# Performance work log

Hardware: AMD Instinct MI355X
Metric: run time of the kernel (lower is better)

Reference implementation:

```python
import jax, jax.numpy as jnp
import numpy as np

BATCH, IN_F, OUT_F = 4096, 1024, 1024


def setup_inputs() -> dict:
    key = jax.random.key(0)
    kx, kw = jax.random.split(key)
    x = jax.random.normal(kx, (BATCH, IN_F, 4), dtype=jnp.float32)
    weight = jax.random.normal(kw, (OUT_F, IN_F, 4), dtype=jnp.float32) * 0.01
    bias = jnp.zeros((OUT_F, 4), dtype=jnp.float32)
    return {"x": x, "weight": weight, "bias": bias}


def reference(x, weight, bias):
    # x: (batch, in, 4) quaternions; weight: (out, in, 4); bias: (out, 4)
    # Hamilton product broadcast over (batch, out, in) then summed over in ==
    # 16 signed real GEMMs contracting the `in` dimension.
    ar, ai, aj, ak = x[..., 0], x[..., 1], x[..., 2], x[..., 3]          # (b, i)
    br, bi, bj, bk = weight[..., 0], weight[..., 1], weight[..., 2], weight[..., 3]  # (o, i)

    mm = lambda a, w: jnp.einsum('bi,oi->bo', a, w)

    out_r = mm(ar, br) - mm(ai, bi) - mm(aj, bj) - mm(ak, bk)
    out_i = mm(ar, bi) + mm(ai, br) + mm(aj, bk) - mm(ak, bj)
    out_j = mm(ar, bj) - mm(ai, bk) + mm(aj, br) + mm(ak, bi)
    out_k = mm(ar, bk) + mm(ai, bj) - mm(aj, bi) + mm(ak, br)

    out = jnp.stack([out_r, out_i, out_j, out_k], axis=-1)  # (b, o, 4)
    return out + bias
```

## Files before the change

kernel.cpp:

```cpp
#include <hip/hip_runtime.h>


typedef __bf16 bf16x8 __attribute__((ext_vector_type(8)));
typedef float floatx4 __attribute__((ext_vector_type(4)));

constexpr int M = 4096;
constexpr int N = 4096;
constexpr int K = 4096;
constexpr int BM = 256, BN = 256, BK = 64;
constexpr int TILES = K / BK;

constexpr int CVT_BLOCKS = (M * K / 8) / 256;
constexpr int EXP_BLOCKS = (1024 * 1024 / 2) / 256;

#define BARRIER() asm volatile("s_barrier" ::: "memory")
#define SB()      __builtin_amdgcn_sched_barrier(0)
#define LGKM0()   do { asm volatile("s_waitcnt lgkmcnt(0)"); SB(); } while (0)
#define LGKM4()   do { asm volatile("s_waitcnt lgkmcnt(4)"); SB(); } while (0)
#define LDS_OFF(p) ((unsigned)(uintptr_t)(__attribute__((address_space(3))) const void*)(p))

__global__ void prep_kernel(const float* __restrict__ x, const float* __restrict__ w,
                            __bf16* __restrict__ A, __bf16* __restrict__ Wb) {
    const int b = blockIdx.x;
    if (b < CVT_BLOCKS) {
        const size_t i = (size_t)b * 256 + threadIdx.x;
        const float4* xp = (const float4*)x;
        float4 a = xp[2 * i];
        float4 c = xp[2 * i + 1];
        bf16x8 v;
        v[0] = (__bf16)a.x; v[1] = (__bf16)a.y; v[2] = (__bf16)a.z; v[3] = (__bf16)a.w;
        v[4] = (__bf16)c.x; v[5] = (__bf16)c.y; v[6] = (__bf16)c.z; v[7] = (__bf16)c.w;
        *(bf16x8*)(A + 8 * i) = v;
    } else {
        const int idx = (b - CVT_BLOCKS) * 256 + threadIdx.x;
        const int o  = idx >> 9;
        const int ip = (idx & 511) * 2;
        float4 q0 = ((const float4*)w)[o * 1024 + ip];
        float4 q1 = ((const float4*)w)[o * 1024 + ip + 1];
        __bf16* base = Wb + (size_t)(o * 4) * K + ip * 4;
        bf16x8 r;
        r[0] = (__bf16)q0.x; r[1] = (__bf16)(-q0.y); r[2] = (__bf16)(-q0.z); r[3] = (__bf16)(-q0.w);
        r[4] = (__bf16)q1.x; r[5] = (__bf16)(-q1.y); r[6] = (__bf16)(-q1.z); r[7] = (__bf16)(-q1.w);
        *(bf16x8*)(base) = r;
        r[0] = (__bf16)q0.y; r[1] = (__bf16)q0.x; r[2] = (__bf16)q0.w; r[3] = (__bf16)(-q0.z);
        r[4] = (__bf16)q1.y; r[5] = (__bf16)q1.x; r[6] = (__bf16)q1.w; r[7] = (__bf16)(-q1.z);
        *(bf16x8*)(base + (size_t)K) = r;
        r[0] = (__bf16)q0.z; r[1] = (__bf16)(-q0.w); r[2] = (__bf16)q0.x; r[3] = (__bf16)q0.y;
        r[4] = (__bf16)q1.z; r[5] = (__bf16)(-q1.w); r[6] = (__bf16)q1.x; r[7] = (__bf16)q1.y;
        *(bf16x8*)(base + (size_t)2 * K) = r;
        r[0] = (__bf16)q0.w; r[1] = (__bf16)q0.z; r[2] = (__bf16)(-q0.y); r[3] = (__bf16)q0.x;
        r[4] = (__bf16)q1.w; r[5] = (__bf16)q1.z; r[6] = (__bf16)(-q1.y); r[7] = (__bf16)q1.x;
        *(bf16x8*)(base + (size_t)3 * K) = r;
    }
}

__device__ __forceinline__ void gload_lds16(const __bf16* g, __bf16* l) {
    __builtin_amdgcn_global_load_lds(
        (const __attribute__((address_space(1))) void*)g,
        (__attribute__((address_space(3))) void*)l, 16, 0, 0);
}

__device__ __forceinline__ bf16x8 dsr128(unsigned addr) {
    bf16x8 r;
    asm volatile("ds_read_b128 %0, %1" : "=v"(r) : "v"(addr));
    return r;
}

__global__ __launch_bounds__(512, 2) void qgemm_kernel(const __bf16* __restrict__ A,
                                                       const __bf16* __restrict__ B,
                                                       const float* __restrict__ bias,
                                                       float* __restrict__ C) {
    __shared__ __bf16 As[2][BM][BK];
    __shared__ __bf16 Bs[2][BN][BK];

    const int tid  = threadIdx.x;
    const int wave = tid >> 6;
    const int lane = tid & 63;

    const int bid = blockIdx.x;
    const int xcd = bid & 7;
    const int q   = bid >> 3;
    const int tm  = (xcd >> 2) * 8 + (q & 7);
    const int tn  = (xcd & 3) * 4 + (q >> 3);
    const int bm  = tm * BM;
    const int bn  = tn * BN;

    const int wm = (wave >> 2) * 128;
    const int wn = (wave & 3) * 64;

    const int srow = wave * 16 + (lane >> 3);
    const int schk = ((lane & 7) ^ (lane >> 3)) * 8;
    const __bf16* agA = A + (size_t)(bm + srow) * K + schk;
    const __bf16* agB = B + (size_t)(bn + srow) * K + schk;

    auto issueA = [&](int buf, int h, int t) {
        const __bf16* g = agA + (size_t)h * 128 * K + t * BK;
        gload_lds16(g,                 &As[buf][h * 128 + wave * 16][0]);
        gload_lds16(g + (size_t)8 * K, &As[buf][h * 128 + wave * 16 + 8][0]);
    };
    auto issueB = [&](int buf, int h, int t) {
        const __bf16* g = agB + (size_t)h * 128 * K + t * BK;
        gload_lds16(g,                 &Bs[buf][h * 128 + wave * 16][0]);
        gload_lds16(g + (size_t)8 * K, &Bs[buf][h * 128 + wave * 16 + 8][0]);
    };

    const int fl  = lane & 15;
    const int fq  = lane >> 4;
    const int fx7 = fl & 7;
    const unsigned ebo0 = (unsigned)(((fq)     ^ fx7) * 16);
    const unsigned ebo1 = (unsigned)(((4 + fq) ^ fx7) * 16);
    const unsigned aRow = LDS_OFF(&As[0][0][0]) + (unsigned)(wm + fl) * 128u;
    const unsigned bRow = LDS_OFF(&Bs[0][0][0]) + (unsigned)(wn + fl) * 128u;

    floatx4 acc[8][4] = {};
    bf16x8 x0, x1, x2, x3, y0, y1, y2, y3;
    bf16x8 bE0, bE1, bE2, bE3, bO0, bO1, bO2, bO3;
    bf16x8 s0, s1, s2, s3;

#define HALF(i0, i1, AA, AB, F0, F1, F2, F3)                                      \
    acc[i0][0] = __builtin_amdgcn_mfma_f32_16x16x32_bf16(AA, F0, acc[i0][0], 0, 0, 0); \
    acc[i1][0] = __builtin_amdgcn_mfma_f32_16x16x32_bf16(AB, F0, acc[i1][0], 0, 0, 0); \
    acc[i0][1] = __builtin_amdgcn_mfma_f32_16x16x32_bf16(AA, F1, acc[i0][1], 0, 0, 0); \
    acc[i1][1] = __builtin_amdgcn_mfma_f32_16x16x32_bf16(AB, F1, acc[i1][1], 0, 0, 0); \
    acc[i0][2] = __builtin_amdgcn_mfma_f32_16x16x32_bf16(AA, F2, acc[i0][2], 0, 0, 0); \
    acc[i1][2] = __builtin_amdgcn_mfma_f32_16x16x32_bf16(AB, F2, acc[i1][2], 0, 0, 0); \
    acc[i0][3] = __builtin_amdgcn_mfma_f32_16x16x32_bf16(AA, F3, acc[i0][3], 0, 0, 0); \
    acc[i1][3] = __builtin_amdgcn_mfma_f32_16x16x32_bf16(AB, F3, acc[i1][3], 0, 0, 0)

#define TILE(T, BUFC, BC0, BC1, BC2, BC3, BX0, BX1, BX2, BX3, ISSB)               \
    do {                                                                          \
        const unsigned bsc_ = (BUFC) * 32768u;                                    \
        const unsigned bsn_ = (1 - (BUFC)) * 32768u;                              \
                \
        issueA(1 - (BUFC), 0, (T) + 1); issueA(1 - (BUFC), 1, (T) + 1);           \
        s0 = dsr128(bRow + bsc_ + 0u    + ebo1);                                  \
        s1 = dsr128(bRow + bsc_ + 2048u + ebo1);                                  \
        s2 = dsr128(bRow + bsc_ + 4096u + ebo1);                                  \
        s3 = dsr128(bRow + bsc_ + 6144u + ebo1);                                  \
        y0 = dsr128(aRow + bsc_ + 4096u + ebo0);                                  \
        y1 = dsr128(aRow + bsc_ + 4096u + ebo1);                                  \
        y2 = dsr128(aRow + bsc_ + 6144u + ebo0);                                  \
        y3 = dsr128(aRow + bsc_ + 6144u + ebo1);                                  \
        SB();                                                                     \
        __builtin_amdgcn_s_setprio(1);                                            \
        HALF(0, 1, x0, x2, BC0, BC1, BC2, BC3);                                   \
        __builtin_amdgcn_s_setprio(0);                                            \
        LGKM4();                                    \
        __builtin_amdgcn_s_setprio(1);                                            \
        HALF(0, 1, x1, x3, s0, s1, s2, s3);                                       \
        __builtin_amdgcn_s_setprio(0);                                            \
        LGKM0();                                                                  \
              \
        x0 = dsr128(aRow + bsc_ + 8192u  + ebo0);                                 \
        x1 = dsr128(aRow + bsc_ + 8192u  + ebo1);                                 \
        x2 = dsr128(aRow + bsc_ + 10240u + ebo0);                                 \
        x3 = dsr128(aRow + bsc_ + 10240u + ebo1);                                 \
        SB();                                                                     \
        __builtin_amdgcn_s_setprio(1);                                            \
        HALF(2, 3, y0, y2, BC0, BC1, BC2, BC3);                                   \
        HALF(2, 3, y1, y3, s0, s1, s2, s3);                                       \
        __builtin_amdgcn_s_setprio(0);                                            \
        LGKM0();                                                                  \
        asm volatile("s_waitcnt vmcnt(0)");       \
        BARRIER();                                        \
        if (ISSB) { issueB((BUFC), 0, (T) + 2); issueB((BUFC), 1, (T) + 2); }     \
                 \
        y0 = dsr128(aRow + bsc_ + 12288u + ebo0);                                 \
        y1 = dsr128(aRow + bsc_ + 12288u + ebo1);                                 \
        y2 = dsr128(aRow + bsc_ + 14336u + ebo0);                                 \
        y3 = dsr128(aRow + bsc_ + 14336u + ebo1);                                 \
        BX0 = dsr128(bRow + bsn_ + 0u    + ebo0);                                 \
        BX1 = dsr128(bRow + bsn_ + 2048u + ebo0);                                 \
        BX2 = dsr128(bRow + bsn_ + 4096u + ebo0);                                 \
        BX3 = dsr128(bRow + bsn_ + 6144u + ebo0);                                 \
        SB();                                                                     \
        __builtin_amdgcn_s_setprio(1);                                            \
        HALF(4, 5, x0, x2, BC0, BC1, BC2, BC3);                                   \
        HALF(4, 5, x1, x3, s0, s1, s2, s3);                                       \
        __builtin_amdgcn_s_setprio(0);                                            \
        LGKM4();                                   \
                            \
        x0 = dsr128(aRow + bsn_ + 0u    + ebo0);                                  \
        x1 = dsr128(aRow + bsn_ + 0u    + ebo1);                                  \
        x2 = dsr128(aRow + bsn_ + 2048u + ebo0);                                  \
        x3 = dsr128(aRow + bsn_ + 2048u + ebo1);                                  \
        SB();                                                                     \
        __builtin_amdgcn_s_setprio(1);                                            \
        HALF(6, 7, y0, y2, BC0, BC1, BC2, BC3);                                   \
        HALF(6, 7, y1, y3, s0, s1, s2, s3);                                       \
        __builtin_amdgcn_s_setprio(0);                                            \
        LGKM0();                                         \
        BARRIER();                               \
    } while (0)

    issueB(0, 0, 0); issueB(0, 1, 0);
    issueA(0, 0, 0); issueA(0, 1, 0);
    issueB(1, 0, 1); issueB(1, 1, 1);
    asm volatile("s_waitcnt vmcnt(4)");
    BARRIER();
    bE0 = dsr128(bRow + 0u    + ebo0);
    bE1 = dsr128(bRow + 2048u + ebo0);
    bE2 = dsr128(bRow + 4096u + ebo0);
    bE3 = dsr128(bRow + 6144u + ebo0);
    x0  = dsr128(aRow + 0u    + ebo0);
    x1  = dsr128(aRow + 0u    + ebo1);
    x2  = dsr128(aRow + 2048u + ebo0);
    x3  = dsr128(aRow + 2048u + ebo1);
    LGKM0();

    for (int t = 0; t < 62; t += 2) {
        TILE(t,     0, bE0, bE1, bE2, bE3, bO0, bO1, bO2, bO3, true);
        TILE(t + 1, 1, bO0, bO1, bO2, bO3, bE0, bE1, bE2, bE3, true);
    }
    TILE(62, 0, bE0, bE1, bE2, bE3, bO0, bO1, bO2, bO3, false);

    {
        const unsigned bsc_ = 32768u;
        s0 = dsr128(bRow + bsc_ + 0u    + ebo1);
        s1 = dsr128(bRow + bsc_ + 2048u + ebo1);
        s2 = dsr128(bRow + bsc_ + 4096u + ebo1);
        s3 = dsr128(bRow + bsc_ + 6144u + ebo1);
        y0 = dsr128(aRow + bsc_ + 4096u + ebo0);
        y1 = dsr128(aRow + bsc_ + 4096u + ebo1);
        y2 = dsr128(aRow + bsc_ + 6144u + ebo0);
        y3 = dsr128(aRow + bsc_ + 6144u + ebo1);
        SB();
        __builtin_amdgcn_s_setprio(1);
        HALF(0, 1, x0, x2, bO0, bO1, bO2, bO3);
        __builtin_amdgcn_s_setprio(0);
        LGKM4();
        __builtin_amdgcn_s_setprio(1);
        HALF(0, 1, x1, x3, s0, s1, s2, s3);
        __builtin_amdgcn_s_setprio(0);
        LGKM0();
        x0 = dsr128(aRow + bsc_ + 8192u  + ebo0);
        x1 = dsr128(aRow + bsc_ + 8192u  + ebo1);
        x2 = dsr128(aRow + bsc_ + 10240u + ebo0);
        x3 = dsr128(aRow + bsc_ + 10240u + ebo1);
        SB();
        __builtin_amdgcn_s_setprio(1);
        HALF(2, 3, y0, y2, bO0, bO1, bO2, bO3);
        HALF(2, 3, y1, y3, s0, s1, s2, s3);
        __builtin_amdgcn_s_setprio(0);
        LGKM0();
        y0 = dsr128(aRow + bsc_ + 12288u + ebo0);
        y1 = dsr128(aRow + bsc_ + 12288u + ebo1);
        y2 = dsr128(aRow + bsc_ + 14336u + ebo0);
        y3 = dsr128(aRow + bsc_ + 14336u + ebo1);
        SB();
        __builtin_amdgcn_s_setprio(1);
        HALF(4, 5, x0, x2, bO0, bO1, bO2, bO3);
        HALF(4, 5, x1, x3, s0, s1, s2, s3);
        __builtin_amdgcn_s_setprio(0);
        LGKM0();
        __builtin_amdgcn_s_setprio(1);
        HALF(6, 7, y0, y2, bO0, bO1, bO2, bO3);
        HALF(6, 7, y1, y3, s0, s1, s2, s3);
        __builtin_amdgcn_s_setprio(0);
    }

#pragma unroll
    for (int mt = 0; mt < 8; ++mt) {
        const int row = bm + wm + mt * 16 + fq * 4;
#pragma unroll
        for (int nt = 0; nt < 4; ++nt) {
            const int col = bn + wn + nt * 16 + fl;
            const float bv = bias[col];
            float* cp = C + (size_t)row * N + col;
#pragma unroll
            for (int r = 0; r < 4; ++r)
                cp[(size_t)r * N] = acc[mt][nt][r] + bv;
        }
    }
#undef TILE
#undef HALF
}

extern "C" void kernel_launch(void* const* d_in, const int* in_sizes, int n_in,
                              void* d_out, int out_size, void* d_ws, size_t ws_size,
                              hipStream_t stream) {
    const float* x    = (const float*)d_in[0];
    const float* w    = (const float*)d_in[1];
    const float* bias = (const float*)d_in[2];
    float* out = (float*)d_out;

    __bf16* Abf  = (__bf16*)d_ws;
    __bf16* Wbig = (__bf16*)((char*)d_ws + (size_t)M * K * 2);

    prep_kernel<<<CVT_BLOCKS + EXP_BLOCKS, 256, 0, stream>>>(x, w, Abf, Wbig);

    qgemm_kernel<<<256, 512, 0, stream>>>(Abf, Wbig, bias, out);
}
```

Before: 286.5 us.

## Triple-buffer A tiles in LDS with deeper prefetch and immediate-offset LDS reads

Expands the A shared-memory buffer from two stages to three so A tiles are prefetched two iterations ahead. The mid-tile global-load wait becomes a partial vmcnt instead of a full drain, so loads can stay in flight across the barrier. LDS reads now use the ds_read immediate offset field on precomputed per-buffer base addresses, which cuts per-read address arithmetic. The main loop is unrolled by six to rotate the buffers, at the cost of more LDS (160KB per block) and more live VGPRs.

```diff
diff --git a/kernel.cpp b/kernel.cpp
--- a/kernel.cpp
+++ b/kernel.cpp
@@ -8,7 +8,6 @@
 constexpr int N = 4096;
 constexpr int K = 4096;
 constexpr int BM = 256, BN = 256, BK = 64;
-constexpr int TILES = K / BK;
 
 constexpr int CVT_BLOCKS = (M * K / 8) / 256;
 constexpr int EXP_BLOCKS = (1024 * 1024 / 2) / 256;
@@ -60,9 +59,10 @@
         (__attribute__((address_space(3))) void*)l, 16, 0, 0);
 }
 
-__device__ __forceinline__ bf16x8 dsr128(unsigned addr) {
+template <int OFF>
+__device__ __forceinline__ bf16x8 dsrO(unsigned base) {
     bf16x8 r;
-    asm volatile("ds_read_b128 %0, %1" : "=v"(r) : "v"(addr));
+    asm volatile("ds_read_b128 %0, %1 offset:%c2" : "=v"(r) : "v"(base), "i"(OFF));
     return r;
 }
 
@@ -70,7 +70,7 @@
                                                        const __bf16* __restrict__ B,
                                                        const float* __restrict__ bias,
                                                        float* __restrict__ C) {
-    __shared__ __bf16 As[2][BM][BK];
+    __shared__ __bf16 As[3][BM][BK];
     __shared__ __bf16 Bs[2][BN][BK];
 
     const int tid  = threadIdx.x;
@@ -109,15 +109,25 @@
     const int fx7 = fl & 7;
     const unsigned ebo0 = (unsigned)(((fq)     ^ fx7) * 16);
     const unsigned ebo1 = (unsigned)(((4 + fq) ^ fx7) * 16);
-    const unsigned aRow = LDS_OFF(&As[0][0][0]) + (unsigned)(wm + fl) * 128u;
-    const unsigned bRow = LDS_OFF(&Bs[0][0][0]) + (unsigned)(wn + fl) * 128u;
+    const unsigned aR0  = LDS_OFF(&As[0][0][0]) + (unsigned)(wm + fl) * 128u + ebo0;
+    const unsigned aR1  = LDS_OFF(&As[0][0][0]) + (unsigned)(wm + fl) * 128u + ebo1;
+    const unsigned aR0b1 = aR0 + 32768u, aR1b1 = aR1 + 32768u;
+    const unsigned aR0b2 = aR0 + 65536u, aR1b2 = aR1 + 65536u;
+    const unsigned bR0  = LDS_OFF(&Bs[0][0][0]) + (unsigned)(wn + fl) * 128u + ebo0;
+    const unsigned bR1  = LDS_OFF(&Bs[0][0][0]) + (unsigned)(wn + fl) * 128u + ebo1;
+    const unsigned bR0b1 = bR0 + 32768u, bR1b1 = bR1 + 32768u;
 
     floatx4 acc[8][4] = {};
-    bf16x8 x0, x1, x2, x3, y0, y1, y2, y3;
-    bf16x8 bE0, bE1, bE2, bE3, bO0, bO1, bO2, bO3;
+    bf16x8 x0, x1, x2, x3;
+    bf16x8 y0, y1, y2, y3;
+    bf16x8 w0, w1, w2, w3;
+    bf16x8 z0, z1, z2, z3;
     bf16x8 s0, s1, s2, s3;
-
-#define HALF(i0, i1, AA, AB, F0, F1, F2, F3)                                      \
+    bf16x8 c0, c1, c2, c3;
+    bf16x8 d0, d1, d2, d3;
+    bf16x8 n0, n1, n2, n3;
+
+#define HALFK(i0, i1, AA, AB, F0, F1, F2, F3)                                     \
     acc[i0][0] = __builtin_amdgcn_mfma_f32_16x16x32_bf16(AA, F0, acc[i0][0], 0, 0, 0); \
     acc[i1][0] = __builtin_amdgcn_mfma_f32_16x16x32_bf16(AB, F0, acc[i1][0], 0, 0, 0); \
     acc[i0][1] = __builtin_amdgcn_mfma_f32_16x16x32_bf16(AA, F1, acc[i0][1], 0, 0, 0); \
@@ -127,135 +137,117 @@
     acc[i0][3] = __builtin_amdgcn_mfma_f32_16x16x32_bf16(AA, F3, acc[i0][3], 0, 0, 0); \
     acc[i1][3] = __builtin_amdgcn_mfma_f32_16x16x32_bf16(AB, F3, acc[i1][3], 0, 0, 0)
 
-#define TILE(T, BUFC, BC0, BC1, BC2, BC3, BX0, BX1, BX2, BX3, ISSB)               \
+#define TILE(T, A0c, A1c, A0n, A1n, B0c, B1c, B0x, DA, DB, ISSA, ISSB, MIDVM)     \
     do {                                                                          \
-        const unsigned bsc_ = (BUFC) * 32768u;                                    \
-        const unsigned bsn_ = (1 - (BUFC)) * 32768u;                              \
-                \
-        issueA(1 - (BUFC), 0, (T) + 1); issueA(1 - (BUFC), 1, (T) + 1);           \
-        s0 = dsr128(bRow + bsc_ + 0u    + ebo1);                                  \
-        s1 = dsr128(bRow + bsc_ + 2048u + ebo1);                                  \
-        s2 = dsr128(bRow + bsc_ + 4096u + ebo1);                                  \
-        s3 = dsr128(bRow + bsc_ + 6144u + ebo1);                                  \
-        y0 = dsr128(aRow + bsc_ + 4096u + ebo0);                                  \
-        y1 = dsr128(aRow + bsc_ + 4096u + ebo1);                                  \
-        y2 = dsr128(aRow + bsc_ + 6144u + ebo0);                                  \
-        y3 = dsr128(aRow + bsc_ + 6144u + ebo1);                                  \
-        SB();                                                                     \
-        __builtin_amdgcn_s_setprio(1);                                            \
-        HALF(0, 1, x0, x2, BC0, BC1, BC2, BC3);                                   \
-        __builtin_amdgcn_s_setprio(0);                                            \
-        LGKM4();                                    \
-        __builtin_amdgcn_s_setprio(1);                                            \
-        HALF(0, 1, x1, x3, s0, s1, s2, s3);                                       \
-        __builtin_amdgcn_s_setprio(0);                                            \
-        LGKM0();                                                                  \
+                      \
+        if (ISSA) { issueA(DA, 0, (T) + 2); issueA(DA, 1, (T) + 2); }             \
+        s0 = dsrO<0>(B1c); s1 = dsrO<2048>(B1c);                                  \
+        s2 = dsrO<4096>(B1c); s3 = dsrO<6144>(B1c);                               \
+        y0 = dsrO<4096>(A0c); y1 = dsrO<4096>(A1c);                               \
+        y2 = dsrO<6144>(A0c); y3 = dsrO<6144>(A1c);                               \
+        SB();                                                                     \
+        __builtin_amdgcn_s_setprio(1);                                            \
+        HALFK(0, 1, x0, x2, c0, c1, c2, c3);                                      \
+        __builtin_amdgcn_s_setprio(0);                                            \
+        LGKM4();                                       \
+        __builtin_amdgcn_s_setprio(1);                                            \
+        HALFK(0, 1, x1, x3, s0, s1, s2, s3);                                      \
+        __builtin_amdgcn_s_setprio(0);                                            \
+                     \
+        w0 = dsrO<8192>(A0c); w1 = dsrO<8192>(A1c);                               \
+        w2 = dsrO<10240>(A0c); w3 = dsrO<10240>(A1c);                             \
+        SB();                                                                     \
+        LGKM4();                                       \
+        __builtin_amdgcn_s_setprio(1);                                            \
+        HALFK(2, 3, y0, y2, c0, c1, c2, c3);                                      \
+        HALFK(2, 3, y1, y3, s0, s1, s2, s3);                                      \
+        __builtin_amdgcn_s_setprio(0);                                            \
+        LGKM0();                                                      \
+        asm volatile("s_waitcnt vmcnt(" #MIDVM ")");    \
+        BARRIER();                                        \
+        if (ISSB) { issueB(DB, 0, (T) + 2); issueB(DB, 1, (T) + 2); }             \
               \
-        x0 = dsr128(aRow + bsc_ + 8192u  + ebo0);                                 \
-        x1 = dsr128(aRow + bsc_ + 8192u  + ebo1);                                 \
-        x2 = dsr128(aRow + bsc_ + 10240u + ebo0);                                 \
-        x3 = dsr128(aRow + bsc_ + 10240u + ebo1);                                 \
-        SB();                                                                     \
-        __builtin_amdgcn_s_setprio(1);                                            \
-        HALF(2, 3, y0, y2, BC0, BC1, BC2, BC3);                                   \
-        HALF(2, 3, y1, y3, s0, s1, s2, s3);                                       \
-        __builtin_amdgcn_s_setprio(0);                                            \
-        LGKM0();                                                                  \
-        asm volatile("s_waitcnt vmcnt(0)");       \
-        BARRIER();                                        \
-        if (ISSB) { issueB((BUFC), 0, (T) + 2); issueB((BUFC), 1, (T) + 2); }     \
-                 \
-        y0 = dsr128(aRow + bsc_ + 12288u + ebo0);                                 \
-        y1 = dsr128(aRow + bsc_ + 12288u + ebo1);                                 \
-        y2 = dsr128(aRow + bsc_ + 14336u + ebo0);                                 \
-        y3 = dsr128(aRow + bsc_ + 14336u + ebo1);                                 \
-        BX0 = dsr128(bRow + bsn_ + 0u    + ebo0);                                 \
-        BX1 = dsr128(bRow + bsn_ + 2048u + ebo0);                                 \
-        BX2 = dsr128(bRow + bsn_ + 4096u + ebo0);                                 \
-        BX3 = dsr128(bRow + bsn_ + 6144u + ebo0);                                 \
-        SB();                                                                     \
-        __builtin_amdgcn_s_setprio(1);                                            \
-        HALF(4, 5, x0, x2, BC0, BC1, BC2, BC3);                                   \
-        HALF(4, 5, x1, x3, s0, s1, s2, s3);                                       \
-        __builtin_amdgcn_s_setprio(0);                                            \
-        LGKM4();                                   \
-                            \
-        x0 = dsr128(aRow + bsn_ + 0u    + ebo0);                                  \
-        x1 = dsr128(aRow + bsn_ + 0u    + ebo1);                                  \
-        x2 = dsr128(aRow + bsn_ + 2048u + ebo0);                                  \
-        x3 = dsr128(aRow + bsn_ + 2048u + ebo1);                                  \
-        SB();                                                                     \
-        __builtin_amdgcn_s_setprio(1);                                            \
-        HALF(6, 7, y0, y2, BC0, BC1, BC2, BC3);                                   \
-        HALF(6, 7, y1, y3, s0, s1, s2, s3);                                       \
-        __builtin_amdgcn_s_setprio(0);                                            \
-        LGKM0();                                         \
-        BARRIER();                               \
+        z0 = dsrO<12288>(A0c); z1 = dsrO<12288>(A1c);                             \
+        z2 = dsrO<14336>(A0c); z3 = dsrO<14336>(A1c);                             \
+        d0 = dsrO<0>(B0x); d1 = dsrO<2048>(B0x);                                  \
+        d2 = dsrO<4096>(B0x); d3 = dsrO<6144>(B0x);                               \
+        SB();                                                                     \
+        __builtin_amdgcn_s_setprio(1);                                            \
+        HALFK(4, 5, w0, w2, c0, c1, c2, c3);                                      \
+        HALFK(4, 5, w1, w3, s0, s1, s2, s3);                                      \
+        __builtin_amdgcn_s_setprio(0);                                            \
+                                        \
+        LGKM4();                                       \
+        n0 = dsrO<0>(A0n); n1 = dsrO<0>(A1n);                                     \
+        n2 = dsrO<2048>(A0n); n3 = dsrO<2048>(A1n);                               \
+        SB();                                                                     \
+        __builtin_amdgcn_s_setprio(1);                                            \
+        HALFK(6, 7, z0, z2, c0, c1, c2, c3);                                      \
+        HALFK(6, 7, z1, z3, s0, s1, s2, s3);                                      \
+        __builtin_amdgcn_s_setprio(0);                                            \
+        LGKM0();                          \
+        BARRIER();                                               \
+        x0 = n0; x1 = n1; x2 = n2; x3 = n3;                                       \
+        c0 = d0; c1 = d1; c2 = d2; c3 = d3;                                       \
     } while (0)
 
     issueB(0, 0, 0); issueB(0, 1, 0);
     issueA(0, 0, 0); issueA(0, 1, 0);
     issueB(1, 0, 1); issueB(1, 1, 1);
-    asm volatile("s_waitcnt vmcnt(4)");
+    issueA(1, 0, 1); issueA(1, 1, 1);
+    asm volatile("s_waitcnt vmcnt(0)");
     BARRIER();
-    bE0 = dsr128(bRow + 0u    + ebo0);
-    bE1 = dsr128(bRow + 2048u + ebo0);
-    bE2 = dsr128(bRow + 4096u + ebo0);
-    bE3 = dsr128(bRow + 6144u + ebo0);
-    x0  = dsr128(aRow + 0u    + ebo0);
-    x1  = dsr128(aRow + 0u    + ebo1);
-    x2  = dsr128(aRow + 2048u + ebo0);
-    x3  = dsr128(aRow + 2048u + ebo1);
+    x0 = dsrO<0>(aR0);    x1 = dsrO<0>(aR1);
+    x2 = dsrO<2048>(aR0); x3 = dsrO<2048>(aR1);
+    c0 = dsrO<0>(bR0);    c1 = dsrO<2048>(bR0);
+    c2 = dsrO<4096>(bR0); c3 = dsrO<6144>(bR0);
     LGKM0();
 
-    for (int t = 0; t < 62; t += 2) {
-        TILE(t,     0, bE0, bE1, bE2, bE3, bO0, bO1, bO2, bO3, true);
-        TILE(t + 1, 1, bO0, bO1, bO2, bO3, bE0, bE1, bE2, bE3, true);
-    }
-    TILE(62, 0, bE0, bE1, bE2, bE3, bO0, bO1, bO2, bO3, false);
+    for (int t = 0; t < 60; t += 6) {
+        TILE(t + 0, aR0,   aR1,   aR0b1, aR1b1, bR0,   bR1,   bR0b1, 2, 0, true, true, 4);
+        TILE(t + 1, aR0b1, aR1b1, aR0b2, aR1b2, bR0b1, bR1b1, bR0,   0, 1, true, true, 4);
+        TILE(t + 2, aR0b2, aR1b2, aR0,   aR1,   bR0,   bR1,   bR0b1, 1, 0, true, true, 4);
+        TILE(t + 3, aR0,   aR1,   aR0b1, aR1b1, bR0b1, bR1b1, bR0,   2, 1, true, true, 4);
+        TILE(t + 4, aR0b1, aR1b1, aR0b2, aR1b2, bR0,   bR1,   bR0b1, 0, 0, true, true, 4);
+        TILE(t + 5, aR0b2, aR1b2, aR0,   aR1,   bR0b1, bR1b1, bR0,   1, 1, true, true, 4);
+    }
+    TILE(60, aR0,   aR1,   aR0b1, aR1b1, bR0,   bR1,   bR0b1, 2, 0, true,  true,  4);
+    TILE(61, aR0b1, aR1b1, aR0b2, aR1b2, bR0b1, bR1b1, bR0,   0, 1, true,  true,  4);
+    TILE(62, aR0b2, aR1b2, aR0,   aR1,   bR0,   bR1,   bR0b1, 1, 0, false, false, 0);
 
     {
-        const unsigned bsc_ = 32768u;
-        s0 = dsr128(bRow + bsc_ + 0u    + ebo1);
-        s1 = dsr128(bRow + bsc_ + 2048u + ebo1);
-        s2 = dsr128(bRow + bsc_ + 4096u + ebo1);
-        s3 = dsr128(bRow + bsc_ + 6144u + ebo1);
-        y0 = dsr128(aRow + bsc_ + 4096u + ebo0);
-        y1 = dsr128(aRow + bsc_ + 4096u + ebo1);
-        y2 = dsr128(aRow + bsc_ + 6144u + ebo0);
-        y3 = dsr128(aRow + bsc_ + 6144u + ebo1);
+        s0 = dsrO<0>(bR1b1); s1 = dsrO<2048>(bR1b1);
+        s2 = dsrO<4096>(bR1b1); s3 = dsrO<6144>(bR1b1);
+        y0 = dsrO<4096>(aR0); y1 = dsrO<4096>(aR1);
+        y2 = dsrO<6144>(aR0); y3 = dsrO<6144>(aR1);
         SB();
         __builtin_amdgcn_s_setprio(1);
-        HALF(0, 1, x0, x2, bO0, bO1, bO2, bO3);
+        HALFK(0, 1, x0, x2, c0, c1, c2, c3);
         __builtin_amdgcn_s_setprio(0);
         LGKM4();
         __builtin_amdgcn_s_setprio(1);
-        HALF(0, 1, x1, x3, s0, s1, s2, s3);
+        HALFK(0, 1, x1, x3, s0, s1, s2, s3);
+        __builtin_amdgcn_s_setprio(0);
+        w0 = dsrO<8192>(aR0); w1 = dsrO<8192>(aR1);
+        w2 = dsrO<10240>(aR0); w3 = dsrO<10240>(aR1);
+        SB();
+        LGKM4();
+        __builtin_amdgcn_s_setprio(1);
+        HALFK(2, 3, y0, y2, c0, c1, c2, c3);
+        HALFK(2, 3, y1, y3, s0, s1, s2, s3);
         __builtin_amdgcn_s_setprio(0);
         LGKM0();
-        x0 = dsr128(aRow + bsc_ + 8192u  + ebo0);
-        x1 = dsr128(aRow + bsc_ + 8192u  + ebo1);
-        x2 = dsr128(aRow + bsc_ + 10240u + ebo0);
-        x3 = dsr128(aRow + bsc_ + 10240u + ebo1);
+        z0 = dsrO<12288>(aR0); z1 = dsrO<12288>(aR1);
+        z2 = dsrO<14336>(aR0); z3 = dsrO<14336>(aR1);
         SB();
         __builtin_amdgcn_s_setprio(1);
-        HALF(2, 3, y0, y2, bO0, bO1, bO2, bO3);
-        HALF(2, 3, y1, y3, s0, s1, s2, s3);
+        HALFK(4, 5, w0, w2, c0, c1, c2, c3);
+        HALFK(4, 5, w1, w3, s0, s1, s2, s3);
         __builtin_amdgcn_s_setprio(0);
         LGKM0();
-        y0 = dsr128(aRow + bsc_ + 12288u + ebo0);
-        y1 = dsr128(aRow + bsc_ + 12288u + ebo1);
-        y2 = dsr128(aRow + bsc_ + 14336u + ebo0);
-        y3 = dsr128(aRow + bsc_ + 14336u + ebo1);
-        SB();
-        __builtin_amdgcn_s_setprio(1);
-        HALF(4, 5, x0, x2, bO0, bO1, bO2, bO3);
-        HALF(4, 5, x1, x3, s0, s1, s2, s3);
-        __builtin_amdgcn_s_setprio(0);
-        LGKM0();
-        __builtin_amdgcn_s_setprio(1);
-        HALF(6, 7, y0, y2, bO0, bO1, bO2, bO3);
-        HALF(6, 7, y1, y3, s0, s1, s2, s3);
+        __builtin_amdgcn_s_setprio(1);
+        HALFK(6, 7, z0, z2, c0, c1, c2, c3);
+        HALFK(6, 7, z1, z3, s0, s1, s2, s3);
         __builtin_amdgcn_s_setprio(0);
     }
 
@@ -273,7 +265,7 @@
         }
     }
 #undef TILE
-#undef HALF
+#undef HALFK
 }
 
 extern "C" void kernel_launch(void* const* d_in, const int* in_sizes, int n_in,
```

Measured after the change: 235.9 us. 17.7% less time.
